# Kernel tuning notes

Hardware: AMD Instinct MI355X
Metric: run time of the kernel (lower is better)

The kernel has to match this reference:

```python
import jax, jax.numpy as jnp
import numpy as np

N_NODES = 100000
N_EDGES = 1600000
HID = 128
BOND = 16
BN_EPS = 1e-5


def setup_inputs() -> dict:
    key = jax.random.key(0)
    ks = jax.random.split(key, 12)
    sb = 1.0 / np.sqrt(BOND)
    sh = 1.0 / np.sqrt(HID)
    return {
        "features": jax.random.normal(ks[0], (N_NODES, HID), jnp.float32),
        "edge_feats": jax.random.normal(ks[1], (N_EDGES, BOND), jnp.float32),
        "src": jax.random.randint(ks[2], (N_EDGES,), 0, N_NODES, jnp.int32),
        "dst": jax.random.randint(ks[3], (N_EDGES,), 0, N_NODES, jnp.int32),
        "Wb": jax.random.uniform(ks[4], (HID, BOND), jnp.float32, -sb, sb),
        "bb": jax.random.uniform(ks[5], (HID,), jnp.float32, -sb, sb),
        "W1": jax.random.uniform(ks[6], (HID, HID), jnp.float32, -sh, sh),
        "b1": jax.random.uniform(ks[7], (HID,), jnp.float32, -sh, sh),
        "W2": jax.random.uniform(ks[8], (HID, HID), jnp.float32, -sh, sh),
        "b2": jax.random.uniform(ks[9], (HID,), jnp.float32, -sh, sh),
        "gamma1": jnp.ones((HID,), jnp.float32),
        "beta1": jnp.zeros((HID,), jnp.float32),
        "gamma2": jnp.ones((HID,), jnp.float32),
        "beta2": jnp.zeros((HID,), jnp.float32),
    }


def _batchnorm(x, gamma, beta):
    # BatchNorm1d in training mode: normalize with batch stats (biased var).
    mean = jnp.mean(x, axis=0)
    var = jnp.var(x, axis=0)
    return (x - mean) * jax.lax.rsqrt(var + BN_EPS) * gamma + beta


def reference(features, edge_feats, src, dst, Wb, bb, W1, b1, W2, b2,
              gamma1, beta1, gamma2, beta2):
    n = features.shape[0]
    # edge linear: [E, BOND] -> [E, HID]
    eh = edge_feats @ Wb.T + bb
    # mailbox sums: sum of src node features and edge messages per dst node
    h1 = jax.ops.segment_sum(features[src], dst, num_segments=n)  # [N, HID]
    h2 = jax.ops.segment_sum(eh, dst, num_segments=n)             # [N, HID]
    h = jax.nn.relu(_batchnorm(h1 @ W1.T + b1 + h2, gamma1, beta1))
    h = jax.nn.relu(_batchnorm(h @ W2.T + b2 + features, gamma2, beta2))
    return h
```

## Files before the change

kernel.cpp:

```cpp
#include <hip/hip_runtime.h>

#define NN 100000
#define NE 1600000
#define HID 128
#define KEXT 160
#define ROWB 320
#define BSH 9
#define BNODES 512
#define NB 196
#define P2B 2048
#define EPB2 782
#define SCAP 10240
#define NROWP 100096
#define GGRID 782
#define BN_EPS 1e-5f

typedef __attribute__((ext_vector_type(8))) short bf16x8;
typedef __attribute__((ext_vector_type(4))) float f32x4;

__device__ inline unsigned short f2bf(float x) {
  union { float f; unsigned u; } v; v.f = x;
  unsigned r = v.u + 0x7FFFu + ((v.u >> 16) & 1u);
  return (unsigned short)(r >> 16);
}
__device__ inline unsigned pk2(float a, float b) {
  return (unsigned)f2bf(a) | ((unsigned)f2bf(b) << 16);
}
__device__ inline float bflo(unsigned p) { return __uint_as_float(p << 16); }
__device__ inline float bfhi(unsigned p) { return __uint_as_float(p & 0xffff0000u); }

__device__ inline void gload_lds16(const void* g, void* l) {
  __builtin_amdgcn_global_load_lds((const __attribute__((address_space(1))) void*)g,
                                   (__attribute__((address_space(3))) void*)l, 16, 0, 0);
}

__global__ __launch_bounds__(256) void fbw_k(const float* __restrict__ f,
                                             unsigned* __restrict__ fb,
                                             const float* __restrict__ W1,
                                             const float* __restrict__ Wb,
                                             const float* __restrict__ bb,
                                             const float* __restrict__ b1,
                                             const float* __restrict__ W2,
                                             unsigned short* __restrict__ W1e,
                                             unsigned short* __restrict__ W2e,
                                             const int* __restrict__ dst,
                                             int* __restrict__ cnts_s) {
  __shared__ int bh[NB];
  if (blockIdx.x < 25000) {
    int i = blockIdx.x * 256 + threadIdx.x;
    float2 v = ((const float2*)f)[i];
    fb[i] = pk2(v.x, v.y);
  } else if (blockIdx.x < 25080) {
    int idx = (blockIdx.x - 25000) * 256 + threadIdx.x;
    if (idx < 128 * KEXT) {
      int c = idx / KEXT, k = idx - c * KEXT;
      float v1 = 0.f;
      if (k < 128) v1 = W1[c * HID + k];
      else if (k < 144) v1 = Wb[c * 16 + (k - 128)];
      else if (k == 144) v1 = bb[c];
      else if (k == 145) v1 = b1[c];
      W1e[idx] = f2bf(v1);
    }
    if (idx < 128 * 128) W2e[idx] = f2bf(W2[(idx >> 7) * HID + (idx & 127)]);
  } else {
    int blk = blockIdx.x - 25080;
    int b0 = blk * EPB2, e1 = min(b0 + EPB2, NE);
    for (int i = threadIdx.x; i < NB; i += 256) bh[i] = 0;
    __syncthreads();
    for (int e = b0 + threadIdx.x; e < e1; e += 256) atomicAdd(&bh[dst[e] >> BSH], 1);
    __syncthreads();
    for (int i = threadIdx.x; i < NB; i += 256) cnts_s[i * P2B + blk] = bh[i];
  }
}

__global__ __launch_bounds__(1024) void cscan_k(int* __restrict__ cnts_s,
                                                int* __restrict__ bcnt_s,
                                                int* __restrict__ bcnt_r) {
  __shared__ int s[1024];
  int b = blockIdx.x, t = threadIdx.x;
  int x0 = cnts_s[b * P2B + 2 * t];
  int x1 = cnts_s[b * P2B + 2 * t + 1];
  int xs0 = (x0 + 1) & ~1;
  int xs1 = (x1 + 1) & ~1;
  s[t] = xs0 + xs1; __syncthreads();
  for (int off = 1; off < 1024; off <<= 1) {
    int v = (t >= off) ? s[t - off] : 0; __syncthreads();
    s[t] += v; __syncthreads();
  }
  int exclp = s[t] - (xs0 + xs1);
  cnts_s[b * P2B + 2 * t] = exclp;
  cnts_s[b * P2B + 2 * t + 1] = exclp + xs0;
  if (t == 1023) bcnt_s[b] = s[1023];
  __syncthreads();
  s[t] = x0 + x1; __syncthreads();
  for (int off = 1; off < 1024; off <<= 1) {
    int v = (t >= off) ? s[t - off] : 0; __syncthreads();
    s[t] += v; __syncthreads();
  }
  if (t == 1023) bcnt_r[b] = s[1023];
}

__global__ __launch_bounds__(256) void bscan_k(const int* __restrict__ bcnt_r,
                                               const int* __restrict__ bcnt_s,
                                               int* __restrict__ bbase_r,
                                               int* __restrict__ bbase_s,
                                               int* __restrict__ rs) {
  __shared__ int s[256];
  int t = threadIdx.x;
#pragma unroll
  for (int pass = 0; pass < 2; ++pass) {
    const int* in = (pass == 0) ? bcnt_r : bcnt_s;
    int* out = (pass == 0) ? bbase_r : bbase_s;
    int x = (t < NB) ? in[t] : 0;
    s[t] = x; __syncthreads();
    for (int off = 1; off < 256; off <<= 1) {
      int v = (t >= off) ? s[t - off] : 0; __syncthreads();
      s[t] += v; __syncthreads();
    }
    if (t < NB) out[t] = s[t] - x;
    if (t == NB - 1) out[NB] = s[t];
    __syncthreads();
  }
  if (t == 0) rs[NN] = NE;
}

__global__ __launch_bounds__(256) void part3_k(const int* __restrict__ src,
                                               const int* __restrict__ dst,
                                               const float* __restrict__ ef,
                                               const int* __restrict__ bbase_s,
                                               const int* __restrict__ cnts_s,
                                               unsigned* __restrict__ stg,
                                               float4* __restrict__ efb) {
  __shared__ int th[NB], ts[NB], cnt2[NB], st_s[NB];
  __shared__ int sscan[256];
  __shared__ unsigned spk[EPB2 + 1];
  int blk = blockIdx.x, tid = threadIdx.x;
  int b0 = blk * EPB2;
  int tc = min(EPB2, NE - b0);
  if (tc < 0) tc = 0;
  for (int i = tid; i < NB; i += 256) {
    th[i] = 0; cnt2[i] = 0;
    st_s[i] = bbase_s[i] + cnts_s[i * P2B + blk];
  }
  __syncthreads();
  float sink = 0.f;
  for (int le = tid; le < tc; le += 256) {
    int e = b0 + le;
    atomicAdd(&th[dst[e] >> BSH], 1);
    const float4* efp = (const float4*)(ef + (size_t)e * 16);
    float4 a = efp[0], b4 = efp[1], c4 = efp[2], d4 = efp[3];
    sink += a.x + b4.x + c4.x + d4.x;
  }
  asm volatile("" : "+v"(sink));
  __syncthreads();
  sscan[tid] = (tid < NB) ? th[tid] : 0;
  __syncthreads();
  for (int off = 1; off < 256; off <<= 1) {
    int v = (tid >= off) ? sscan[tid - off] : 0;
    __syncthreads();
    sscan[tid] += v;
    __syncthreads();
  }
  if (tid < NB) ts[tid] = sscan[tid] - th[tid];
  __syncthreads();
  for (int le = tid; le < tc; le += 256) {
    int d = dst[b0 + le];
    int b = d >> BSH;
    int slot = ts[b] + atomicAdd(&cnt2[b], 1);
    spk[slot] = ((unsigned)b << 20) | ((unsigned)(d & (BNODES - 1)) << 11) | (unsigned)le;
  }
  __syncthreads();
  for (int s2 = tid; s2 < tc; s2 += 256) {
    unsigned pk = spk[s2];
    int b = pk >> 20, d9 = (pk >> 11) & 511, le = pk & 2047;
    int e = b0 + le;
    int gs = st_s[b] + (s2 - ts[b]);
    stg[gs] = (unsigned)src[e] | ((unsigned)d9 << 17) | (1u << 26);
    const float4* efp = (const float4*)(ef + (size_t)e * 16);
    float4 a = efp[0], b4 = efp[1], c4 = efp[2], d4 = efp[3];
    float4 w0, w1;
    w0.x = __uint_as_float(pk2(a.x, a.y));   w0.y = __uint_as_float(pk2(a.z, a.w));
    w0.z = __uint_as_float(pk2(b4.x, b4.y)); w0.w = __uint_as_float(pk2(b4.z, b4.w));
    w1.x = __uint_as_float(pk2(c4.x, c4.y)); w1.y = __uint_as_float(pk2(c4.z, c4.w));
    w1.z = __uint_as_float(pk2(d4.x, d4.y)); w1.w = __uint_as_float(pk2(d4.z, d4.w));
    efb[(size_t)gs * 2] = w0;
    efb[(size_t)gs * 2 + 1] = w1;
  }
  __syncthreads();
  for (int i = tid; i < NB; i += 256) {
    int c = th[i];
    if (c & 1) stg[st_s[i] + c] = 0u;
  }
}

__global__ __launch_bounds__(512) void bsort_k(const unsigned* __restrict__ stg,
                                               const int* __restrict__ bbase_s,
                                               const int* __restrict__ bbase_r,
                                               const unsigned* __restrict__ efbu,
                                               int* __restrict__ rs,
                                               unsigned* __restrict__ fin,
                                               unsigned* __restrict__ efsum) {
  __shared__ int h[BNODES], sc[BNODES], cur[BNODES];
  __shared__ int tot;
  __shared__ unsigned slds[SCAP];
  int b = blockIdx.x, n0 = b << BSH, tid = threadIdx.x;
  int s0p = bbase_s[b], e1p = bbase_s[b + 1];
  int s0r = bbase_r[b];
  h[tid] = 0;
  __syncthreads();
  for (int i = s0p + tid; i < e1p; i += 512) {
    unsigned rec = stg[i];
    if (rec >> 26) atomicAdd(&h[(rec >> 17) & (BNODES - 1)], 1);
  }
  __syncthreads();
  sc[tid] = h[tid];
  __syncthreads();
  for (int off = 1; off < BNODES; off <<= 1) {
    int v = (tid >= off) ? sc[tid - off] : 0;
    __syncthreads();
    sc[tid] += v;
    __syncthreads();
  }
  int excl = sc[tid] - h[tid];
  cur[tid] = excl;
  int n = n0 + tid;
  if (n < NN) rs[n] = s0r + excl;
  if (tid == BNODES - 1) tot = sc[tid];
  __syncthreads();
  for (int i = s0p + tid; i < e1p; i += 512) {
    unsigned rec = stg[i];
    if (rec >> 26) {
      int d = (rec >> 17) & (BNODES - 1);
      int p = atomicAdd(&cur[d], 1);
      slds[p] = (rec & 0x1FFFF) | ((unsigned)(i - s0p) << 17);
    }
  }
  __syncthreads();
  int T = tot;
  for (int j = tid; j < T; j += 512) fin[s0r + j] = slds[j] & 0x1FFFF;
  if (n < NN) {
    float a[16];
#pragma unroll
    for (int k = 0; k < 16; ++k) a[k] = 0.f;
    for (int j = excl; j < sc[tid]; ++j) {
      unsigned rec = slds[j];
      const unsigned* ep = efbu + ((size_t)s0p + (rec >> 17)) * 8;
#pragma unroll
      for (int k = 0; k < 8; ++k) {
        unsigned u = ep[k];
        a[2 * k] += bflo(u);
        a[2 * k + 1] += bfhi(u);
      }
    }
    unsigned* op = efsum + (size_t)n * 8;
#pragma unroll
    for (int k = 0; k < 8; ++k) op[k] = pk2(a[2 * k], a[2 * k + 1]);
  }
}

__global__ __launch_bounds__(256) void feg_k(const unsigned* __restrict__ fb,
                                             const int* __restrict__ rs,
                                             const unsigned* __restrict__ fin,
                                             const unsigned* __restrict__ efsum,
                                             unsigned short* __restrict__ A1) {
  int bid = (int)(blockIdx.x & 7) * 3125 + (int)(blockIdx.x >> 3);
  int wid = threadIdx.x >> 6, lane = threadIdx.x & 63;
  int node = bid * 4 + wid;
  if (node >= NN) return;
  int start = rs[node], end = rs[node + 1];
  float ax0 = 0.f, ay0 = 0.f, ax1 = 0.f, ay1 = 0.f;
  float ax2 = 0.f, ay2 = 0.f, ax3 = 0.f, ay3 = 0.f;
  float ax4 = 0.f, ay4 = 0.f, ax5 = 0.f, ay5 = 0.f;
  float ax6 = 0.f, ay6 = 0.f, ax7 = 0.f, ay7 = 0.f;
  int i = start;
  for (; i + 8 <= end; i += 8) {
    int sl = 0;
    if (lane < 8) sl = (int)fin[i + lane];
    int s0 = __shfl(sl, 0), s1 = __shfl(sl, 1), s2 = __shfl(sl, 2), s3 = __shfl(sl, 3);
    int s4 = __shfl(sl, 4), s5 = __shfl(sl, 5), s6 = __shfl(sl, 6), s7 = __shfl(sl, 7);
    unsigned p0 = fb[s0 * 64 + lane];
    unsigned p1 = fb[s1 * 64 + lane];
    unsigned p2 = fb[s2 * 64 + lane];
    unsigned p3 = fb[s3 * 64 + lane];
    unsigned p4 = fb[s4 * 64 + lane];
    unsigned p5 = fb[s5 * 64 + lane];
    unsigned p6 = fb[s6 * 64 + lane];
    unsigned p7 = fb[s7 * 64 + lane];
    ax0 += bflo(p0); ay0 += bfhi(p0);
    ax1 += bflo(p1); ay1 += bfhi(p1);
    ax2 += bflo(p2); ay2 += bfhi(p2);
    ax3 += bflo(p3); ay3 += bfhi(p3);
    ax4 += bflo(p4); ay4 += bfhi(p4);
    ax5 += bflo(p5); ay5 += bfhi(p5);
    ax6 += bflo(p6); ay6 += bfhi(p6);
    ax7 += bflo(p7); ay7 += bfhi(p7);
  }
  for (; i < end; ++i) {
    int sl = 0;
    if (lane == 0) sl = (int)fin[i];
    int s0 = __shfl(sl, 0);
    unsigned p0 = fb[s0 * 64 + lane];
    ax0 += bflo(p0); ay0 += bfhi(p0);
  }
  float ax = ((ax0 + ax1) + (ax2 + ax3)) + ((ax4 + ax5) + (ax6 + ax7));
  float ay = ((ay0 + ay1) + (ay2 + ay3)) + ((ay4 + ay5) + (ay6 + ay7));
  char* rowp = (char*)A1 + (size_t)node * ROWB;
  *(unsigned*)(rowp + lane * 4) = pk2(ax, ay);
  if (lane < 8) {
    *(unsigned*)(rowp + 256 + 4 * lane) = efsum[(size_t)node * 8 + lane];
  } else if (lane < 16) {
    int j2 = lane - 8;
    *(unsigned*)(rowp + 288 + 4 * j2) =
        (j2 == 0) ? pk2((float)(end - start), 1.0f) : 0u;
  }
}

__global__ __launch_bounds__(256) void gemm1_k(
    const unsigned short* __restrict__ A, const unsigned short* __restrict__ W,
    unsigned short* __restrict__ outb, float* __restrict__ statsP) {
  __shared__ __align__(16) char sA[128 * ROWB];
  __shared__ __align__(16) char sW[128 * ROWB];
  const int tid = threadIdx.x;
  const int wid = tid >> 6, lane = tid & 63;
  const size_t r0 = (size_t)blockIdx.x * 128;

#pragma unroll
  for (int q = 0; q < 10; ++q) {
    int s = q * 256 + tid;
    int row = (s * 3277) >> 16;
    int c = s - row * 20;
    int csrc = (c < 16) ? (c ^ (row & 7)) : (16 + ((c - 16) ^ (row & 3)));
    gload_lds16((const char*)A + (r0 + row) * ROWB + csrc * 16,
                sA + (size_t)(q * 256 + wid * 64) * 16);
  }
#pragma unroll
  for (int q = 0; q < 10; ++q) {
    int s = q * 256 + tid;
    int row = (s * 3277) >> 16;
    int c = s - row * 20;
    int csrc = (c < 16) ? (c ^ (row & 7)) : (16 + ((c - 16) ^ (row & 3)));
    gload_lds16((const char*)W + (size_t)row * ROWB + csrc * 16,
                sW + (size_t)(q * 256 + wid * 64) * 16);
  }
  __syncthreads();

  const int l15 = lane & 15;
  const int kgr = lane >> 4;
  bf16x8 afrag[2][5];
#pragma unroll
  for (int rt = 0; rt < 2; ++rt) {
    int arow = wid * 32 + rt * 16 + l15;
#pragma unroll
    for (int ks = 0; ks < 5; ++ks) {
      int creq = ks * 4 + kgr;
      int csw = (creq < 16) ? (creq ^ (arow & 7)) : (16 + ((creq - 16) ^ (arow & 3)));
      afrag[rt][ks] = *(const bf16x8*)(sA + arow * ROWB + csw * 16);
    }
  }
  f32x4 acc[2][8];
#pragma unroll
  for (int rt = 0; rt < 2; ++rt)
#pragma unroll
    for (int ct = 0; ct < 8; ++ct) acc[rt][ct] = (f32x4){0.f, 0.f, 0.f, 0.f};
#pragma unroll
  for (int ct = 0; ct < 8; ++ct) {
    int brow = ct * 16 + l15;
#pragma unroll
    for (int ks = 0; ks < 5; ++ks) {
      int creq = ks * 4 + kgr;
      int csw = (creq < 16) ? (creq ^ (brow & 7)) : (16 + ((creq - 16) ^ (brow & 3)));
      bf16x8 bfrag = *(const bf16x8*)(sW + brow * ROWB + csw * 16);
      acc[0][ct] = __builtin_amdgcn_mfma_f32_16x16x32_bf16(afrag[0][ks], bfrag, acc[0][ct], 0, 0, 0);
      acc[1][ct] = __builtin_amdgcn_mfma_f32_16x16x32_bf16(afrag[1][ks], bfrag, acc[1][ct], 0, 0, 0);
    }
  }

  float cs[8], cq[8];
#pragma unroll
  for (int ct = 0; ct < 8; ++ct) { cs[ct] = 0.f; cq[ct] = 0.f; }
#pragma unroll
  for (int rt = 0; rt < 2; ++rt) {
    const size_t orow0 = r0 + wid * 32 + rt * 16 + kgr * 4;
#pragma unroll
    for (int ct = 0; ct < 8; ++ct) {
      int col = ct * 16 + l15;
#pragma unroll
      for (int r = 0; r < 4; ++r) {
        size_t row = orow0 + r;
        if (row < NN) {
          float v = acc[rt][ct][r];
          outb[row * HID + col] = f2bf(v);
          cs[ct] += v; cq[ct] += v * v;
        }
      }
    }
  }
#pragma unroll
  for (int ct = 0; ct < 8; ++ct) {
    cs[ct] += __shfl_xor(cs[ct], 16); cs[ct] += __shfl_xor(cs[ct], 32);
    cq[ct] += __shfl_xor(cq[ct], 16); cq[ct] += __shfl_xor(cq[ct], 32);
  }
  __syncthreads();
  float* red = (float*)sA;
  if (lane < 16) {
#pragma unroll
    for (int ct = 0; ct < 8; ++ct) {
      red[wid * 256 + ct * 16 + l15] = cs[ct];
      red[wid * 256 + 128 + ct * 16 + l15] = cq[ct];
    }
  }
  __syncthreads();
  if (tid < 256) {
    float* base = statsP + (size_t)(blockIdx.x & 15) * 512;
    float s_ = red[tid] + red[256 + tid] + red[512 + tid] + red[768 + tid];
    atomicAdd(&base[tid], s_);
  }
}

__global__ void bnred_k(const float* __restrict__ statsP, int base,
                        const float* __restrict__ gamma, const float* __restrict__ beta,
                        float* __restrict__ scale, float* __restrict__ shift) {
  int c = threadIdx.x;
  if (c < 128) {
    float s_ = 0.f, q_ = 0.f;
#pragma unroll
    for (int i = 0; i < 16; ++i) {
      s_ += statsP[i * 512 + base + c];
      q_ += statsP[i * 512 + base + 128 + c];
    }
    const float invN = 1.f / (float)NN;
    float m = s_ * invN;
    float var = q_ * invN - m * m;
    float inv = rsqrtf(var + BN_EPS);
    float sc = gamma[c] * inv;
    scale[c] = sc;
    shift[c] = beta[c] - m * sc;
  }
}

__global__ __launch_bounds__(256) void gemm2_k(
    const unsigned* __restrict__ t, const unsigned short* __restrict__ W,
    const float* __restrict__ scale, const float* __restrict__ shift,
    const float* __restrict__ b2, const unsigned* __restrict__ fbres,
    unsigned short* __restrict__ outb, float* __restrict__ statsP) {
  __shared__ __align__(16) char sA[128 * 256];
  __shared__ __align__(16) char sW[128 * 256];
  __shared__ float ssc[128], ssh[128];
  const int tid = threadIdx.x;
  const int wid = tid >> 6, lane = tid & 63;
  const size_t r0 = (size_t)blockIdx.x * 128;

  if (tid < 128) {
    ssc[tid] = scale[tid];
    ssh[tid] = shift[tid];
  }
#pragma unroll
  for (int q = 0; q < 8; ++q) {
    int s = q * 256 + tid;
    int row = s >> 4, c = s & 15;
    int csrc = c ^ (row & 7);
    gload_lds16((const char*)W + (size_t)row * 256 + csrc * 16,
                sW + (size_t)(q * 256 + wid * 64) * 16);
  }
  __syncthreads();

#pragma unroll
  for (int q = 0; q < 8; ++q) {
    int s = q * 256 + tid;
    int sr = s >> 4, c = s & 15;
    size_t grow = r0 + sr;
    uint4 v = make_uint4(0, 0, 0, 0);
    if (grow < NN) v = *(const uint4*)(t + grow * 64 + c * 4);
    int k = c * 8;
    unsigned o0 = pk2(fmaxf(0.f, fmaf(bflo(v.x), ssc[k + 0], ssh[k + 0])),
                      fmaxf(0.f, fmaf(bfhi(v.x), ssc[k + 1], ssh[k + 1])));
    unsigned o1 = pk2(fmaxf(0.f, fmaf(bflo(v.y), ssc[k + 2], ssh[k + 2])),
                      fmaxf(0.f, fmaf(bfhi(v.y), ssc[k + 3], ssh[k + 3])));
    unsigned o2 = pk2(fmaxf(0.f, fmaf(bflo(v.z), ssc[k + 4], ssh[k + 4])),
                      fmaxf(0.f, fmaf(bfhi(v.z), ssc[k + 5], ssh[k + 5])));
    unsigned o3 = pk2(fmaxf(0.f, fmaf(bflo(v.w), ssc[k + 6], ssh[k + 6])),
                      fmaxf(0.f, fmaf(bfhi(v.w), ssc[k + 7], ssh[k + 7])));
    int csw = c ^ (sr & 7);
    uint4 w4; w4.x = o0; w4.y = o1; w4.z = o2; w4.w = o3;
    *(uint4*)(sA + sr * 256 + csw * 16) = w4;
  }
  __syncthreads();

  const int l15 = lane & 15;
  const int kgr = lane >> 4;
  bf16x8 afrag[2][4];
#pragma unroll
  for (int rt = 0; rt < 2; ++rt) {
    int arow = wid * 32 + rt * 16 + l15;
#pragma unroll
    for (int ks = 0; ks < 4; ++ks) {
      int creq = ks * 4 + kgr;
      int csw = creq ^ (arow & 7);
      afrag[rt][ks] = *(const bf16x8*)(sA + arow * 256 + csw * 16);
    }
  }
  f32x4 acc[2][8];
#pragma unroll
  for (int rt = 0; rt < 2; ++rt)
#pragma unroll
    for (int ct = 0; ct < 8; ++ct) acc[rt][ct] = (f32x4){0.f, 0.f, 0.f, 0.f};
#pragma unroll
  for (int ct = 0; ct < 8; ++ct) {
    int brow = ct * 16 + l15;
#pragma unroll
    for (int ks = 0; ks < 4; ++ks) {
      int creq = ks * 4 + kgr;
      int csw = creq ^ (brow & 7);
      bf16x8 bfrag = *(const bf16x8*)(sW + brow * 256 + csw * 16);
      acc[0][ct] = __builtin_amdgcn_mfma_f32_16x16x32_bf16(afrag[0][ks], bfrag, acc[0][ct], 0, 0, 0);
      acc[1][ct] = __builtin_amdgcn_mfma_f32_16x16x32_bf16(afrag[1][ks], bfrag, acc[1][ct], 0, 0, 0);
    }
  }

  float cs[8], cq[8];
#pragma unroll
  for (int ct = 0; ct < 8; ++ct) { cs[ct] = 0.f; cq[ct] = 0.f; }
#pragma unroll
  for (int rt = 0; rt < 2; ++rt) {
    const size_t orow0 = r0 + wid * 32 + rt * 16 + kgr * 4;
#pragma unroll
    for (int ct = 0; ct < 8; ++ct) {
      int col = ct * 16 + l15;
      float b2v = b2[col];
      int ci = col >> 1, par = col & 1;
#pragma unroll
      for (int r = 0; r < 4; ++r) {
        size_t row = orow0 + r;
        if (row < NN) {
          unsigned u = fbres[row * 64 + ci];
          float resid = par ? bfhi(u) : bflo(u);
          float v = acc[rt][ct][r] + b2v + resid;
          outb[row * HID + col] = f2bf(v);
          cs[ct] += v; cq[ct] += v * v;
        }
      }
    }
  }
#pragma unroll
  for (int ct = 0; ct < 8; ++ct) {
    cs[ct] += __shfl_xor(cs[ct], 16); cs[ct] += __shfl_xor(cs[ct], 32);
    cq[ct] += __shfl_xor(cq[ct], 16); cq[ct] += __shfl_xor(cq[ct], 32);
  }
  __syncthreads();
  float* red = (float*)sA;
  if (lane < 16) {
#pragma unroll
    for (int ct = 0; ct < 8; ++ct) {
      red[wid * 256 + ct * 16 + l15] = cs[ct];
      red[wid * 256 + 128 + ct * 16 + l15] = cq[ct];
    }
  }
  __syncthreads();
  if (tid < 256) {
    float* base = statsP + (size_t)(blockIdx.x & 15) * 512 + 256;
    float s_ = red[tid] + red[256 + tid] + red[512 + tid] + red[768 + tid];
    atomicAdd(&base[tid], s_);
  }
}

__global__ __launch_bounds__(256) void bn_final_k(const unsigned* __restrict__ t,
                                                  const float* __restrict__ scale,
                                                  const float* __restrict__ shift,
                                                  float* __restrict__ o) {
  __shared__ float ssc[128], ssh[128];
  int tid = threadIdx.x;
  if (tid < 128) { ssc[tid] = scale[tid]; ssh[tid] = shift[tid]; }
  __syncthreads();
  int i = blockIdx.x * 256 + tid;
  if (i >= NN * 64) return;
  unsigned p = t[i];
  int c = (i & 63) * 2;
  float2 v;
  v.x = fmaxf(0.f, fmaf(bflo(p), ssc[c], ssh[c]));
  v.y = fmaxf(0.f, fmaf(bfhi(p), ssc[c + 1], ssh[c + 1]));
  ((float2*)o)[i] = v;
}

extern "C" void kernel_launch(void* const* d_in, const int* in_sizes, int n_in,
                              void* d_out, int out_size, void* d_ws, size_t ws_size,
                              hipStream_t stream) {
  (void)in_sizes; (void)n_in; (void)out_size; (void)ws_size;
  const float* features   = (const float*)d_in[0];
  const float* edge_feats = (const float*)d_in[1];
  const int*   src        = (const int*)d_in[2];
  const int*   dst        = (const int*)d_in[3];
  const float* Wb         = (const float*)d_in[4];
  const float* bb         = (const float*)d_in[5];
  const float* W1         = (const float*)d_in[6];
  const float* b1         = (const float*)d_in[7];
  const float* W2         = (const float*)d_in[8];
  const float* b2         = (const float*)d_in[9];
  const float* gamma1     = (const float*)d_in[10];
  const float* beta1      = (const float*)d_in[11];
  const float* gamma2     = (const float*)d_in[12];
  const float* beta2      = (const float*)d_in[13];
  float* outp = (float*)d_out;

  char* wsb = (char*)d_ws;
  size_t off = 0;
  auto alloc = [&](size_t nbytes) -> void* {
    off = (off + 255) & ~(size_t)255;
    void* p = wsb + off;
    off += nbytes;
    return p;
  };
  const size_t STGN = (size_t)NE + (size_t)NB * P2B + 64;
  int* row_start = (int*)alloc((size_t)(NN + 1) * 4);
  int* bcnt_r    = (int*)alloc(NB * 4);
  int* bcnt_s    = (int*)alloc(NB * 4);
  int* bbase_r   = (int*)alloc((NB + 1) * 4);
  int* bbase_s   = (int*)alloc((NB + 1) * 4);
  int* cnts_s    = (int*)alloc((size_t)NB * P2B * 4);
  float* statsP  = (float*)alloc(16 * 512 * 4);
  float* scsh    = (float*)alloc(512 * 4);
  unsigned* featb = (unsigned*)alloc((size_t)NN * 64 * 4);
  unsigned short* tbuf = (unsigned short*)alloc((size_t)NROWP * HID * 2);
  unsigned short* A1e = (unsigned short*)alloc((size_t)NROWP * ROWB);
  unsigned short* W1e = (unsigned short*)alloc(128 * KEXT * 2);
  unsigned short* W2e = (unsigned short*)alloc(128 * 128 * 2);
  unsigned* stg  = (unsigned*)alloc(STGN * 4);
  unsigned* fin  = (unsigned*)alloc((size_t)NE * 4);
  float4* efb    = (float4*)alloc(STGN * 32);
  unsigned* efsum = (unsigned*)alloc((size_t)NN * 32);

  hipMemsetAsync(statsP, 0, 16 * 512 * 4, stream);
  hipMemsetAsync((char*)A1e + (size_t)NN * ROWB, 0, (NROWP - NN) * ROWB, stream);

  fbw_k<<<25080 + P2B, 256, 0, stream>>>(features, featb, W1, Wb, bb, b1, W2,
                                         W1e, W2e, dst, cnts_s);
  cscan_k<<<NB, 1024, 0, stream>>>(cnts_s, bcnt_s, bcnt_r);
  bscan_k<<<1, 256, 0, stream>>>(bcnt_r, bcnt_s, bbase_r, bbase_s, row_start);
  part3_k<<<P2B, 256, 0, stream>>>(src, dst, edge_feats, bbase_s, cnts_s, stg, efb);
  bsort_k<<<NB, 512, 0, stream>>>(stg, bbase_s, bbase_r, (const unsigned*)efb,
                                  row_start, fin, efsum);
  feg_k<<<25000, 256, 0, stream>>>(featb, row_start, fin, efsum, A1e);

  gemm1_k<<<GGRID, 256, 0, stream>>>(A1e, W1e, tbuf, statsP);
  bnred_k<<<1, 128, 0, stream>>>(statsP, 0, gamma1, beta1, scsh, scsh + 128);
  gemm2_k<<<GGRID, 256, 0, stream>>>((const unsigned*)tbuf, W2e, scsh, scsh + 128,
                                     b2, featb, tbuf, statsP);
  bnred_k<<<1, 128, 0, stream>>>(statsP, 256, gamma2, beta2, scsh + 256, scsh + 384);
  bn_final_k<<<25000, 256, 0, stream>>>((const unsigned*)tbuf, scsh + 256, scsh + 384,
                                        outp);
}
```

Measured before the change: 292.6 us.

## Decouple edge-feature bf16 conversion from bucket sort and gather edge sums by id

The fp32-to-bf16 conversion of edge features moves into the first fused kernel as a contiguous pass, so part3 no longer reads edge features twice and no longer scatters 32-byte records per edge. Staging records grow to 64 bits and carry the original edge id. bsort now writes the src index and edge id directly to CSR order, and a new efsum_k kernel gathers bf16 edge rows by id to form per-node sums. In exchange it adds a kernel launch, a random gather over the bf16 edge buffer, wider staging records, and padding to multiples of 8.

New measurement: 319.9 us. 1.09x slower.

```diff
diff --git a/kernel.cpp b/kernel.cpp
--- a/kernel.cpp
+++ b/kernel.cpp
@@ -10,13 +10,13 @@
 #define NB 196
 #define P2B 2048
 #define EPB2 782
-#define SCAP 10240
 #define NROWP 100096
 #define GGRID 782
 #define BN_EPS 1e-5f
 
 typedef __attribute__((ext_vector_type(8))) short bf16x8;
 typedef __attribute__((ext_vector_type(4))) float f32x4;
+typedef unsigned long long u64;
 
 __device__ inline unsigned short f2bf(float x) {
   union { float f; unsigned u; } v; v.f = x;
@@ -43,6 +43,8 @@
                                              const float* __restrict__ W2,
                                              unsigned short* __restrict__ W1e,
                                              unsigned short* __restrict__ W2e,
+                                             const float* __restrict__ ef,
+                                             unsigned* __restrict__ efb16,
                                              const int* __restrict__ dst,
                                              int* __restrict__ cnts_s) {
   __shared__ int bh[NB];
@@ -62,8 +64,20 @@
       W1e[idx] = f2bf(v1);
     }
     if (idx < 128 * 128) W2e[idx] = f2bf(W2[(idx >> 7) * HID + (idx & 127)]);
+  } else if (blockIdx.x < 31330) {
+    int e = (blockIdx.x - 25080) * 256 + threadIdx.x;
+    const float4* efp = (const float4*)(ef + (size_t)e * 16);
+    float4 a = efp[0], b4 = efp[1], c4 = efp[2], d4 = efp[3];
+    uint4 w0, w1;
+    w0.x = pk2(a.x, a.y);   w0.y = pk2(a.z, a.w);
+    w0.z = pk2(b4.x, b4.y); w0.w = pk2(b4.z, b4.w);
+    w1.x = pk2(c4.x, c4.y); w1.y = pk2(c4.z, c4.w);
+    w1.z = pk2(d4.x, d4.y); w1.w = pk2(d4.z, d4.w);
+    uint4* op = (uint4*)(efb16 + (size_t)e * 8);
+    op[0] = w0;
+    op[1] = w1;
   } else {
-    int blk = blockIdx.x - 25080;
+    int blk = blockIdx.x - 31330;
     int b0 = blk * EPB2, e1 = min(b0 + EPB2, NE);
     for (int i = threadIdx.x; i < NB; i += 256) bh[i] = 0;
     __syncthreads();
@@ -80,8 +94,8 @@
   int b = blockIdx.x, t = threadIdx.x;
   int x0 = cnts_s[b * P2B + 2 * t];
   int x1 = cnts_s[b * P2B + 2 * t + 1];
-  int xs0 = (x0 + 1) & ~1;
-  int xs1 = (x1 + 1) & ~1;
+  int xs0 = (x0 + 7) & ~7;
+  int xs1 = (x1 + 7) & ~7;
   s[t] = xs0 + xs1; __syncthreads();
   for (int off = 1; off < 1024; off <<= 1) {
     int v = (t >= off) ? s[t - off] : 0; __syncthreads();
@@ -126,11 +140,9 @@
 
 __global__ __launch_bounds__(256) void part3_k(const int* __restrict__ src,
                                                const int* __restrict__ dst,
-                                               const float* __restrict__ ef,
                                                const int* __restrict__ bbase_s,
                                                const int* __restrict__ cnts_s,
-                                               unsigned* __restrict__ stg,
-                                               float4* __restrict__ efb) {
+                                               u64* __restrict__ stg) {
   __shared__ int th[NB], ts[NB], cnt2[NB], st_s[NB];
   __shared__ int sscan[256];
   __shared__ unsigned spk[EPB2 + 1];
@@ -143,15 +155,7 @@
     st_s[i] = bbase_s[i] + cnts_s[i * P2B + blk];
   }
   __syncthreads();
-  float sink = 0.f;
-  for (int le = tid; le < tc; le += 256) {
-    int e = b0 + le;
-    atomicAdd(&th[dst[e] >> BSH], 1);
-    const float4* efp = (const float4*)(ef + (size_t)e * 16);
-    float4 a = efp[0], b4 = efp[1], c4 = efp[2], d4 = efp[3];
-    sink += a.x + b4.x + c4.x + d4.x;
-  }
-  asm volatile("" : "+v"(sink));
+  for (int le = tid; le < tc; le += 256) atomicAdd(&th[dst[b0 + le] >> BSH], 1);
   __syncthreads();
   sscan[tid] = (tid < NB) ? th[tid] : 0;
   __syncthreads();
@@ -175,42 +179,32 @@
     int b = pk >> 20, d9 = (pk >> 11) & 511, le = pk & 2047;
     int e = b0 + le;
     int gs = st_s[b] + (s2 - ts[b]);
-    stg[gs] = (unsigned)src[e] | ((unsigned)d9 << 17) | (1u << 26);
-    const float4* efp = (const float4*)(ef + (size_t)e * 16);
-    float4 a = efp[0], b4 = efp[1], c4 = efp[2], d4 = efp[3];
-    float4 w0, w1;
-    w0.x = __uint_as_float(pk2(a.x, a.y));   w0.y = __uint_as_float(pk2(a.z, a.w));
-    w0.z = __uint_as_float(pk2(b4.x, b4.y)); w0.w = __uint_as_float(pk2(b4.z, b4.w));
-    w1.x = __uint_as_float(pk2(c4.x, c4.y)); w1.y = __uint_as_float(pk2(c4.z, c4.w));
-    w1.z = __uint_as_float(pk2(d4.x, d4.y)); w1.w = __uint_as_float(pk2(d4.z, d4.w));
-    efb[(size_t)gs * 2] = w0;
-    efb[(size_t)gs * 2 + 1] = w1;
+    stg[gs] = (u64)(unsigned)src[e] | ((u64)(unsigned)d9 << 17) | (1ULL << 26) |
+              ((u64)(unsigned)e << 27);
   }
   __syncthreads();
   for (int i = tid; i < NB; i += 256) {
     int c = th[i];
-    if (c & 1) stg[st_s[i] + c] = 0u;
-  }
-}
-
-__global__ __launch_bounds__(512) void bsort_k(const unsigned* __restrict__ stg,
+    int cs = (c + 7) & ~7;
+    for (int j = c; j < cs; ++j) stg[st_s[i] + j] = 0ULL;
+  }
+}
+
+__global__ __launch_bounds__(512) void bsort_k(const u64* __restrict__ stg,
                                                const int* __restrict__ bbase_s,
                                                const int* __restrict__ bbase_r,
-                                               const unsigned* __restrict__ efbu,
                                                int* __restrict__ rs,
                                                unsigned* __restrict__ fin,
-                                               unsigned* __restrict__ efsum) {
+                                               unsigned* __restrict__ eidS) {
   __shared__ int h[BNODES], sc[BNODES], cur[BNODES];
-  __shared__ int tot;
-  __shared__ unsigned slds[SCAP];
   int b = blockIdx.x, n0 = b << BSH, tid = threadIdx.x;
   int s0p = bbase_s[b], e1p = bbase_s[b + 1];
   int s0r = bbase_r[b];
   h[tid] = 0;
   __syncthreads();
   for (int i = s0p + tid; i < e1p; i += 512) {
-    unsigned rec = stg[i];
-    if (rec >> 26) atomicAdd(&h[(rec >> 17) & (BNODES - 1)], 1);
+    u64 rec = stg[i];
+    if ((rec >> 26) & 1) atomicAdd(&h[(int)(rec >> 17) & (BNODES - 1)], 1);
   }
   __syncthreads();
   sc[tid] = h[tid];
@@ -222,40 +216,36 @@
     __syncthreads();
   }
   int excl = sc[tid] - h[tid];
-  cur[tid] = excl;
+  cur[tid] = s0r + excl;
   int n = n0 + tid;
   if (n < NN) rs[n] = s0r + excl;
-  if (tid == BNODES - 1) tot = sc[tid];
   __syncthreads();
   for (int i = s0p + tid; i < e1p; i += 512) {
-    unsigned rec = stg[i];
-    if (rec >> 26) {
-      int d = (rec >> 17) & (BNODES - 1);
+    u64 rec = stg[i];
+    if ((rec >> 26) & 1) {
+      int d = (int)(rec >> 17) & (BNODES - 1);
       int p = atomicAdd(&cur[d], 1);
-      slds[p] = (rec & 0x1FFFF) | ((unsigned)(i - s0p) << 17);
-    }
-  }
-  __syncthreads();
-  int T = tot;
-  for (int j = tid; j < T; j += 512) fin[s0r + j] = slds[j] & 0x1FFFF;
-  if (n < NN) {
-    float a[16];
-#pragma unroll
-    for (int k = 0; k < 16; ++k) a[k] = 0.f;
-    for (int j = excl; j < sc[tid]; ++j) {
-      unsigned rec = slds[j];
-      const unsigned* ep = efbu + ((size_t)s0p + (rec >> 17)) * 8;
-#pragma unroll
-      for (int k = 0; k < 8; ++k) {
-        unsigned u = ep[k];
-        a[2 * k] += bflo(u);
-        a[2 * k + 1] += bfhi(u);
-      }
-    }
-    unsigned* op = efsum + (size_t)n * 8;
-#pragma unroll
-    for (int k = 0; k < 8; ++k) op[k] = pk2(a[2 * k], a[2 * k + 1]);
-  }
+      fin[p] = (unsigned)(rec & 0x1FFFF);
+      eidS[p] = (unsigned)((rec >> 27) & 0x1FFFFF);
+    }
+  }
+}
+
+__global__ __launch_bounds__(256) void efsum_k(const int* __restrict__ rs,
+                                               const unsigned* __restrict__ eidS,
+                                               const unsigned* __restrict__ efb16,
+                                               unsigned* __restrict__ efsum) {
+  int g = threadIdx.x >> 3;
+  int k = threadIdx.x & 7;
+  int n = blockIdx.x * 32 + g;
+  int j0 = rs[n], j1 = rs[n + 1];
+  float a0 = 0.f, a1 = 0.f;
+  for (int j = j0; j < j1; ++j) {
+    int eid = (int)eidS[j];
+    unsigned u = efb16[(size_t)eid * 8 + k];
+    a0 += bflo(u); a1 += bfhi(u);
+  }
+  efsum[(size_t)n * 8 + k] = pk2(a0, a1);
 }
 
 __global__ __launch_bounds__(256) void feg_k(const unsigned* __restrict__ fb,
@@ -609,7 +599,7 @@
     off += nbytes;
     return p;
   };
-  const size_t STGN = (size_t)NE + (size_t)NB * P2B + 64;
+  const size_t STGN = (size_t)NE + 7 * (size_t)NB * P2B + 64;
   int* row_start = (int*)alloc((size_t)(NN + 1) * 4);
   int* bcnt_r    = (int*)alloc(NB * 4);
   int* bcnt_s    = (int*)alloc(NB * 4);
@@ -623,21 +613,22 @@
   unsigned short* A1e = (unsigned short*)alloc((size_t)NROWP * ROWB);
   unsigned short* W1e = (unsigned short*)alloc(128 * KEXT * 2);
   unsigned short* W2e = (unsigned short*)alloc(128 * 128 * 2);
-  unsigned* stg  = (unsigned*)alloc(STGN * 4);
+  u64* stg       = (u64*)alloc(STGN * 8);
   unsigned* fin  = (unsigned*)alloc((size_t)NE * 4);
-  float4* efb    = (float4*)alloc(STGN * 32);
+  unsigned* eidS = (unsigned*)alloc((size_t)NE * 4);
+  unsigned* efb16 = (unsigned*)alloc((size_t)NE * 32);
   unsigned* efsum = (unsigned*)alloc((size_t)NN * 32);
 
   hipMemsetAsync(statsP, 0, 16 * 512 * 4, stream);
   hipMemsetAsync((char*)A1e + (size_t)NN * ROWB, 0, (NROWP - NN) * ROWB, stream);
 
-  fbw_k<<<25080 + P2B, 256, 0, stream>>>(features, featb, W1, Wb, bb, b1, W2,
-                                         W1e, W2e, dst, cnts_s);
+  fbw_k<<<31330 + P2B, 256, 0, stream>>>(features, featb, W1, Wb, bb, b1, W2,
+                                         W1e, W2e, edge_feats, efb16, dst, cnts_s);
   cscan_k<<<NB, 1024, 0, stream>>>(cnts_s, bcnt_s, bcnt_r);
   bscan_k<<<1, 256, 0, stream>>>(bcnt_r, bcnt_s, bbase_r, bbase_s, row_start);
-  part3_k<<<P2B, 256, 0, stream>>>(src, dst, edge_feats, bbase_s, cnts_s, stg, efb);
-  bsort_k<<<NB, 512, 0, stream>>>(stg, bbase_s, bbase_r, (const unsigned*)efb,
-                                  row_start, fin, efsum);
+  part3_k<<<P2B, 256, 0, stream>>>(src, dst, bbase_s, cnts_s, stg);
+  bsort_k<<<NB, 512, 0, stream>>>(stg, bbase_s, bbase_r, row_start, fin, eidS);
+  efsum_k<<<3125, 256, 0, stream>>>(row_start, eidS, efb16, efsum);
   feg_k<<<25000, 256, 0, stream>>>(featb, row_start, fin, efsum, A1e);
 
   gemm1_k<<<GGRID, 256, 0, stream>>>(A1e, W1e, tbuf, statsP);
```
